# Performance work log

Measured on AMD Instinct MI355X. Metric: run time of the kernel, lower is better.

## Reference

```python
import jax, jax.numpy as jnp
import numpy as np

BN_EPS = 1e-5


def setup_inputs() -> dict:
    key = jax.random.key(0)
    ks = jax.random.split(key, 6)
    P, D_IN, H, N_NODES = 2_000_000, 3, 128, 20_000
    x = jax.random.normal(ks[0], (P, D_IN), dtype=jnp.float32)
    batch_idx = jax.random.randint(ks[1], (P,), 0, N_NODES, dtype=jnp.int64)
    W1 = jax.random.normal(ks[2], (D_IN, H), dtype=jnp.float32) * 0.5
    b1 = jax.random.normal(ks[3], (H,), dtype=jnp.float32) * 0.1
    gamma = jnp.ones((H,), dtype=jnp.float32)
    beta = jnp.zeros((H,), dtype=jnp.float32)
    running_mean = jnp.zeros((H,), dtype=jnp.float32)
    running_var = jnp.ones((H,), dtype=jnp.float32)
    W2 = jax.random.normal(ks[4], (H, H), dtype=jnp.float32) * (1.0 / np.sqrt(H))
    b2 = jax.random.normal(ks[5], (H,), dtype=jnp.float32) * 0.1
    return {"x": x, "batch_idx": batch_idx, "num_nodes": N_NODES,
            "W1": W1, "b1": b1, "gamma": gamma, "beta": beta,
            "running_mean": running_mean, "running_var": running_var,
            "W2": W2, "b2": b2}


def reference(x, batch_idx, num_nodes, W1, b1, gamma, beta,
              running_mean, running_var, W2, b2):
    # per-point MLP: Linear -> BatchNorm1d (eval: running stats) -> ReLU -> Linear -> ReLU
    h = x @ W1 + b1                                        # [P, H]
    h = (h - running_mean) * jax.lax.rsqrt(running_var + BN_EPS) * gamma + beta
    h = jax.nn.relu(h)
    h = jax.nn.relu(h @ W2 + b2)                            # [P, H], values >= 0
    # scatter_max by node; torch_scatter fills empty segments with 0,
    # and since h >= 0 post-ReLU, clamping the -inf fill to 0 is exact.
    node_feats = jax.ops.segment_max(h, batch_idx, num_segments=num_nodes)
    return jnp.maximum(node_feats, 0.0)                     # [num_nodes, H]
```

## Files before the change

kernel.cpp:

```cpp
#include <hip/hip_runtime.h>
#include <hip/hip_bf16.h>

#define H 128
#define TILE_PTS 32
#define ROW_STRIDE 136
#define NBLK 192
#define BT 1024
#define BSH 4
#define NPB (1 << BSH)
#define CAP 2048
#define RAWN (CAP + 32)
#define HBUF (TILE_PTS * ROW_STRIDE)

typedef __attribute__((ext_vector_type(8))) short short8;
typedef __attribute__((ext_vector_type(4))) float float4v;
typedef __attribute__((ext_vector_type(2))) float float2v;
typedef __attribute__((ext_vector_type(4))) int int4v;

static __device__ __forceinline__ unsigned short f2bf(float f) {
    unsigned u = __float_as_uint(f);
    unsigned r = (u + 0x7fffu + ((u >> 16) & 1u)) >> 16;
    return (unsigned short)r;
}
static __device__ __forceinline__ unsigned pkbf(float a, float b) {
    __hip_bfloat162 h = __float22bfloat162_rn(float2{a, b});
    return *reinterpret_cast<unsigned*>(&h);
}
static __device__ __forceinline__ unsigned short f2h(float f) {
    _Float16 h = (_Float16)f;
    unsigned short u;
    __builtin_memcpy(&u, &h, 2);
    return u;
}
static __device__ __forceinline__ float h2f(unsigned short us) {
    _Float16 h;
    __builtin_memcpy(&h, &us, 2);
    return (float)h;
}

__global__ __launch_bounds__(BT)
void scatter_slot(const int* __restrict__ bidx, const float* __restrict__ x,
                  const float* __restrict__ W2, unsigned short* __restrict__ W2T,
                  int* __restrict__ gcnt, uint2* __restrict__ xb,
                  int P, int nbuk) {
    extern __shared__ int lh[];
    const int b = blockIdx.x, t = threadIdx.x;
    for (int i = b * BT + t; i < H * H; i += NBLK * BT) {
        int n = i >> 7, k = i & 127;
        W2T[i] = f2bf(W2[k * H + n]);
    }
    for (int i = t; i < nbuk; i += BT) lh[i] = 0;
    __syncthreads();
    const int chunk4 = (((P + NBLK - 1) / NBLK) + 3) & ~3;
    const int lo = b * chunk4;
    const int hi = (lo + chunk4 < P) ? lo + chunk4 : P;
    for (int p4 = lo + 4 * t; p4 < hi; p4 += 4 * BT) {
        if (p4 + 4 <= hi) {
            int4v i4 = *(const int4v*)&bidx[p4];
            atomicAdd(&lh[i4.x >> BSH], 1);
            atomicAdd(&lh[i4.y >> BSH], 1);
            atomicAdd(&lh[i4.z >> BSH], 1);
            atomicAdd(&lh[i4.w >> BSH], 1);
        } else {
            for (int p = p4; p < hi; ++p) atomicAdd(&lh[bidx[p] >> BSH], 1);
        }
    }
    __syncthreads();
    for (int i = t; i < nbuk; i += BT) {
        int c = lh[i];
        lh[i] = (c > 0) ? atomicAdd(&gcnt[i], c) : 0;
    }
    __syncthreads();
    auto emit = [&](int idx, float x0, float x1, float x2) {
        int pos = atomicAdd(&lh[idx >> BSH], 1);
        if (pos < CAP) {
            uint2 r;
            r.x = (unsigned)f2h(x0) | ((unsigned)f2h(x1) << 16);
            r.y = (unsigned)f2h(x2) | ((unsigned)(idx & (NPB - 1)) << 16);
            xb[(size_t)(idx >> BSH) * CAP + pos] = r;
        }
    };
    for (int p4 = lo + 4 * t; p4 < hi; p4 += 4 * BT) {
        if (p4 + 4 <= hi) {
            int4v i4 = *(const int4v*)&bidx[p4];
            float4v xa = *(const float4v*)(x + (size_t)p4 * 3);
            float4v xbv = *(const float4v*)(x + (size_t)p4 * 3 + 4);
            float4v xc = *(const float4v*)(x + (size_t)p4 * 3 + 8);
            emit(i4.x, xa[0], xa[1], xa[2]);
            emit(i4.y, xa[3], xbv[0], xbv[1]);
            emit(i4.z, xbv[2], xbv[3], xc[0]);
            emit(i4.w, xc[1], xc[2], xc[3]);
        } else {
            for (int p = p4; p < hi; ++p)
                emit(bidx[p], x[p * 3 + 0], x[p * 3 + 1], x[p * 3 + 2]);
        }
    }
}

__global__ __launch_bounds__(256, 4)
void node_kernel9(const uint2* __restrict__ xb, const int* __restrict__ gcnt,
                  const float* __restrict__ W1, const float* __restrict__ b1,
                  const float* __restrict__ gamma, const float* __restrict__ beta,
                  const float* __restrict__ rmean, const float* __restrict__ rvar,
                  const unsigned short* __restrict__ W2T, const float* __restrict__ b2,
                  float* __restrict__ out, int N)
{
    __shared__ __align__(16) unsigned short pool[2 * HBUF];
    __shared__ __align__(16) uint2 srt[RAWN];
    __shared__ int basec[NPB + 1];
    __shared__ int cur[NPB];

    const int bk   = blockIdx.x;
    const int t    = threadIdx.x;
    const int lane = t & 63;
    const int wave = t >> 6;
    const int g  = t & 15;
    const int q  = t >> 4;
    const int c0 = g * 8;

    float2v w1f2[3][4], b1f2[4];
    #pragma unroll
    for (int jp = 0; jp < 4; ++jp) {
        #pragma unroll
        for (int e = 0; e < 2; ++e) {
            int c = c0 + 2 * jp + e;
            float sc = gamma[c] * rsqrtf(rvar[c] + 1e-5f);
            w1f2[0][jp][e] = W1[0 * H + c] * sc;
            w1f2[1][jp][e] = W1[1 * H + c] * sc;
            w1f2[2][jp][e] = W1[2 * H + c] * sc;
            b1f2[jp][e]    = (b1[c] - rmean[c]) * sc + beta[c];
        }
    }

    const int bn = lane & 15;
    const int kq = (lane >> 4) * 8;
    short8 bfrag[2][4];
    float  b2v[2];
    #pragma unroll
    for (int nt = 0; nt < 2; ++nt) {
        const int nn = wave * 32 + nt * 16 + bn;
        b2v[nt] = b2[nn];
        #pragma unroll
        for (int kk = 0; kk < 4; ++kk)
            bfrag[nt][kk] = *(const short8*)&W2T[nn * H + kk * 32 + kq];
    }

    uint2* raw = (uint2*)pool;
    int n_b = gcnt[bk];
    if (n_b > CAP) n_b = CAP;
    const uint2* src = xb + (size_t)bk * CAP;
    for (int p = t; p < n_b; p += 256) raw[p] = src[p];
    if (t < NPB) cur[t] = 0;
    __syncthreads();
    for (int p = t; p < n_b; p += 256)
        atomicAdd(&cur[raw[p].y >> 16], 1);
    __syncthreads();
    if (t == 0) {
        int run = 0;
        #pragma unroll
        for (int i = 0; i < NPB; ++i) { int c = cur[i]; basec[i] = run; run += c; }
        basec[NPB] = run;
    }
    __syncthreads();
    if (t < NPB) cur[t] = basec[t];
    __syncthreads();
    for (int p = t; p < n_b; p += 256) {
        uint2 r = raw[p];
        int pos = atomicAdd(&cur[r.y >> 16], 1);
        srt[pos] = r;
    }
    for (int p = n_b + t; p < n_b + TILE_PTS; p += 256)
        if (p < RAWN) srt[p] = uint2{0u, 0u};
    __syncthreads();

    const float4v zero4 = {0.f, 0.f, 0.f, 0.f};
    const float NEG_INF = -__builtin_inff();
    const float2v zero2 = {0.f, 0.f};
    const int nodebase = bk << BSH;
    const int nlocal = (N - nodebase < NPB) ? (N - nodebase) : NPB;

    const int st0 = q * ROW_STRIDE + c0;
    const int st1 = (q + 16) * ROW_STRIDE + c0;
    const int ar  = bn * ROW_STRIDE + kq;

    #define STAGE_PT(r, hs, so)                                            \
    {                                                                      \
        float x0 = h2f((unsigned short)((r).x & 0xffffu));                 \
        float x1 = h2f((unsigned short)((r).x >> 16));                     \
        float x2 = h2f((unsigned short)((r).y & 0xffffu));                 \
        float2v a0 = {x0, x0}, a1 = {x1, x1}, a2 = {x2, x2};               \
        int4v pk;                                                          \
        _Pragma("unroll")                                                  \
        for (int jp = 0; jp < 4; ++jp) {                                   \
            float2v hh = b1f2[jp];                                         \
            hh = __builtin_elementwise_fma(a0, w1f2[0][jp], hh);           \
            hh = __builtin_elementwise_fma(a1, w1f2[1][jp], hh);           \
            hh = __builtin_elementwise_fma(a2, w1f2[2][jp], hh);           \
            hh = __builtin_elementwise_max(hh, zero2);                     \
            pk[jp] = (int)pkbf(hh[0], hh[1]);                              \
        }                                                                  \
        *(int4v*)(void*)&(hs)[so] = pk;                                    \
    }

    for (int j = 0; j < nlocal; ++j) {
        const int startj = basec[j];
        const int n      = basec[j + 1] - startj;
        const int ntiles = (n + TILE_PTS - 1) >> 5;

        float2v vm0 = {NEG_INF, NEG_INF};
        float2v vm1 = {NEG_INF, NEG_INF};

        if (ntiles > 0) {
            unsigned short* hb = pool;
            unsigned short* hs = pool + HBUF;
            {
                uint2 r0 = srt[startj + q];
                uint2 r1 = srt[startj + q + 16];
                STAGE_PT(r0, hb, st0);
                STAGE_PT(r1, hb, st1);
            }
            __syncthreads();

            for (int tile = 0; tile < ntiles; ++tile) {
                const int tb = tile * TILE_PTS;
                const bool have = (tile + 1 < ntiles);

                uint2 n0, n1;
                if (have) {
                    n0 = srt[startj + tb + TILE_PTS + q];
                    n1 = srt[startj + tb + TILE_PTS + 16 + q];
                }

                float4v acc00, acc01, acc10, acc11;
                {
                    short8 a0v = *(const short8*)(const void*)&hb[ar];
                    short8 a1v = *(const short8*)(const void*)&hb[ar + 16 * ROW_STRIDE];
                    acc00 = __builtin_amdgcn_mfma_f32_16x16x32_bf16(a0v, bfrag[0][0], zero4, 0, 0, 0);
                    acc01 = __builtin_amdgcn_mfma_f32_16x16x32_bf16(a0v, bfrag[1][0], zero4, 0, 0, 0);
                    acc10 = __builtin_amdgcn_mfma_f32_16x16x32_bf16(a1v, bfrag[0][0], zero4, 0, 0, 0);
                    acc11 = __builtin_amdgcn_mfma_f32_16x16x32_bf16(a1v, bfrag[1][0], zero4, 0, 0, 0);
                }
                #pragma unroll
                for (int kk = 1; kk < 4; ++kk) {
                    short8 a0v = *(const short8*)(const void*)&hb[ar + kk * 32];
                    short8 a1v = *(const short8*)(const void*)&hb[ar + 16 * ROW_STRIDE + kk * 32];
                    acc00 = __builtin_amdgcn_mfma_f32_16x16x32_bf16(a0v, bfrag[0][kk], acc00, 0, 0, 0);
                    acc01 = __builtin_amdgcn_mfma_f32_16x16x32_bf16(a0v, bfrag[1][kk], acc01, 0, 0, 0);
                    acc10 = __builtin_amdgcn_mfma_f32_16x16x32_bf16(a1v, bfrag[0][kk], acc10, 0, 0, 0);
                    acc11 = __builtin_amdgcn_mfma_f32_16x16x32_bf16(a1v, bfrag[1][kk], acc11, 0, 0, 0);
                }

                if (have) {
                    STAGE_PT(n0, hs, st0);
                    STAGE_PT(n1, hs, st1);
                }

                if (tb + TILE_PTS <= n) {
                    vm0 = __builtin_elementwise_max(vm0, float2v{acc00[0], acc00[1]});
                    vm0 = __builtin_elementwise_max(vm0, float2v{acc00[2], acc00[3]});
                    vm0 = __builtin_elementwise_max(vm0, float2v{acc10[0], acc10[1]});
                    vm0 = __builtin_elementwise_max(vm0, float2v{acc10[2], acc10[3]});
                    vm1 = __builtin_elementwise_max(vm1, float2v{acc01[0], acc01[1]});
                    vm1 = __builtin_elementwise_max(vm1, float2v{acc01[2], acc01[3]});
                    vm1 = __builtin_elementwise_max(vm1, float2v{acc11[0], acc11[1]});
                    vm1 = __builtin_elementwise_max(vm1, float2v{acc11[2], acc11[3]});
                } else {
                    const int r0base = (lane >> 4) * 4;
                    #pragma unroll
                    for (int r = 0; r < 4; ++r) {
                        const bool v0 = (tb + r0base + r) < n;
                        const bool v1 = (tb + 16 + r0base + r) < n;
                        vm0[r & 1] = fmaxf(vm0[r & 1], v0 ? acc00[r] : NEG_INF);
                        vm1[r & 1] = fmaxf(vm1[r & 1], v0 ? acc01[r] : NEG_INF);
                        vm0[r & 1] = fmaxf(vm0[r & 1], v1 ? acc10[r] : NEG_INF);
                        vm1[r & 1] = fmaxf(vm1[r & 1], v1 ? acc11[r] : NEG_INF);
                    }
                }
                __syncthreads();
                unsigned short* tmp = hb; hb = hs; hs = tmp;
            }
        }

        float vmax0 = fmaxf(vm0[0], vm0[1]);
        float vmax1 = fmaxf(vm1[0], vm1[1]);
        vmax0 = fmaxf(vmax0, __shfl_xor(vmax0, 16, 64));
        vmax0 = fmaxf(vmax0, __shfl_xor(vmax0, 32, 64));
        vmax1 = fmaxf(vmax1, __shfl_xor(vmax1, 16, 64));
        vmax1 = fmaxf(vmax1, __shfl_xor(vmax1, 32, 64));
        if (lane < 16) {
            float* orow = out + (size_t)(nodebase + j) * H + wave * 32;
            orow[lane]      = fmaxf(vmax0 + b2v[0], 0.f);
            orow[16 + lane] = fmaxf(vmax1 + b2v[1], 0.f);
        }
    }
    #undef STAGE_PT
}

__global__ void histB_kernel(const int* __restrict__ bidx, int* __restrict__ counts, int P) {
    int p = blockIdx.x * 256 + threadIdx.x;
    if (p < P) atomicAdd(&counts[bidx[p]], 1);
}
__global__ __launch_bounds__(1024)
void scanB_kernel(const int* __restrict__ counts, int* __restrict__ starts,
                  int* __restrict__ cursor, int N) {
    __shared__ int sums[1024];
    const int t = threadIdx.x;
    const int chunk = (N + 1023) >> 10;
    const int lo = t * chunk;
    const int hi = (lo + chunk < N) ? lo + chunk : N;
    int s = 0;
    for (int i = lo; i < hi; ++i) s += counts[i];
    sums[t] = s;
    __syncthreads();
    #pragma unroll
    for (int off = 1; off < 1024; off <<= 1) {
        int a = (t >= off) ? sums[t - off] : 0;
        __syncthreads();
        sums[t] += a;
        __syncthreads();
    }
    int run = sums[t] - s;
    for (int i = lo; i < hi; ++i) { starts[i] = run; cursor[i] = run; run += counts[i]; }
    if (t == 1023) starts[N] = sums[1023];
}
__global__ void scatterB_kernel(const int* __restrict__ bidx, const float* __restrict__ x,
                                int* __restrict__ cursor, uint2* __restrict__ xs, int P) {
    int p = blockIdx.x * 256 + threadIdx.x;
    if (p < P) {
        int pos = atomicAdd(&cursor[bidx[p]], 1);
        uint2 r;
        r.x = (unsigned)f2h(x[p * 3 + 0]) | ((unsigned)f2h(x[p * 3 + 1]) << 16);
        r.y = (unsigned)f2h(x[p * 3 + 2]);
        xs[pos] = r;
    }
}
__global__ void convw2_kernel(const float* __restrict__ W2, unsigned short* __restrict__ W2T) {
    int i = blockIdx.x * 256 + threadIdx.x;
    if (i < H * H) {
        int n = i >> 7, k = i & 127;
        W2T[i] = f2bf(W2[k * H + n]);
    }
}

__global__ __launch_bounds__(256, 4)
void node_kernelB(const uint2* __restrict__ xs,
                  const int*   __restrict__ starts,
                  const float* __restrict__ W1, const float* __restrict__ b1,
                  const float* __restrict__ gamma, const float* __restrict__ beta,
                  const float* __restrict__ rmean, const float* __restrict__ rvar,
                  const unsigned short* __restrict__ W2T, const float* __restrict__ b2,
                  float* __restrict__ out, int N)
{
    __shared__ __align__(16) unsigned short h1s[2][TILE_PTS * ROW_STRIDE];
    const int t = threadIdx.x, lane = t & 63, wave = t >> 6;
    const int g = t & 15, q = t >> 4, c0 = g * 8;
    float2v w1f2[3][4], b1f2[4];
    #pragma unroll
    for (int jp = 0; jp < 4; ++jp)
        #pragma unroll
        for (int e = 0; e < 2; ++e) {
            int c = c0 + 2 * jp + e;
            float sc = gamma[c] * rsqrtf(rvar[c] + 1e-5f);
            w1f2[0][jp][e] = W1[0 * H + c] * sc;
            w1f2[1][jp][e] = W1[1 * H + c] * sc;
            w1f2[2][jp][e] = W1[2 * H + c] * sc;
            b1f2[jp][e]    = (b1[c] - rmean[c]) * sc + beta[c];
        }
    const int bn = lane & 15, kq = (lane >> 4) * 8;
    short8 bfrag[2][4]; float b2v[2];
    #pragma unroll
    for (int nt = 0; nt < 2; ++nt) {
        const int nn = wave * 32 + nt * 16 + bn;
        b2v[nt] = b2[nn];
        #pragma unroll
        for (int kk = 0; kk < 4; ++kk)
            bfrag[nt][kk] = *(const short8*)&W2T[nn * H + kk * 32 + kq];
    }
    const float4v zero4 = {0.f, 0.f, 0.f, 0.f};
    const float NEG_INF = -__builtin_inff();
    const float2v zero2 = {0.f, 0.f};
    for (int node = blockIdx.x; node < N; node += gridDim.x) {
        const int start = starts[node];
        const int n = starts[node + 1] - start;
        const int ntiles = (n + TILE_PTS - 1) >> 5;
        float2v vmax2[2];
        vmax2[0] = float2v{NEG_INF, NEG_INF};
        vmax2[1] = float2v{NEG_INF, NEG_INF};
        auto loadx = [&](int tb, float xv[2][3]) {
            #pragma unroll
            for (int i = 0; i < 2; ++i) {
                uint2 r = xs[start + tb + q + 16 * i];
                xv[i][0] = h2f((unsigned short)(r.x & 0xffffu));
                xv[i][1] = h2f((unsigned short)(r.x >> 16));
                xv[i][2] = h2f((unsigned short)(r.y & 0xffffu));
            }
        };
        auto stage = [&](const float xv[2][3], unsigned short* buf) {
            #pragma unroll
            for (int i = 0; i < 2; ++i) {
                const int pl = q + 16 * i;
                float2v a0 = {xv[i][0], xv[i][0]};
                float2v a1 = {xv[i][1], xv[i][1]};
                float2v a2 = {xv[i][2], xv[i][2]};
                int4v pk;
                #pragma unroll
                for (int jp = 0; jp < 4; ++jp) {
                    float2v h = b1f2[jp];
                    h = __builtin_elementwise_fma(a0, w1f2[0][jp], h);
                    h = __builtin_elementwise_fma(a1, w1f2[1][jp], h);
                    h = __builtin_elementwise_fma(a2, w1f2[2][jp], h);
                    h = __builtin_elementwise_max(h, zero2);
                    pk[jp] = (int)pkbf(h[0], h[1]);
                }
                *(int4v*)(void*)&buf[pl * ROW_STRIDE + c0] = pk;
            }
        };
        if (ntiles > 0) {
            float xv[2][3];
            loadx(0, xv);
            stage(xv, h1s[0]);
            __syncthreads();
            int pb = 0;
            for (int tile = 0; tile < ntiles; ++tile) {
                const int tb = tile * TILE_PTS;
                const bool havenext = (tile + 1 < ntiles);
                float nx[2][3];
                if (havenext) loadx(tb + TILE_PTS, nx);
                float4v acc[2][2];
                const unsigned short* hb = h1s[pb];
                {
                    short8 a0 = *(const short8*)&hb[bn * ROW_STRIDE + kq];
                    short8 a1 = *(const short8*)&hb[(16 + bn) * ROW_STRIDE + kq];
                    #pragma unroll
                    for (int nt = 0; nt < 2; ++nt) {
                        acc[0][nt] = __builtin_amdgcn_mfma_f32_16x16x32_bf16(a0, bfrag[nt][0], zero4, 0, 0, 0);
                        acc[1][nt] = __builtin_amdgcn_mfma_f32_16x16x32_bf16(a1, bfrag[nt][0], zero4, 0, 0, 0);
                    }
                }
                #pragma unroll
                for (int kk = 1; kk < 4; ++kk) {
                    short8 a0 = *(const short8*)&hb[bn * ROW_STRIDE + kk * 32 + kq];
                    short8 a1 = *(const short8*)&hb[(16 + bn) * ROW_STRIDE + kk * 32 + kq];
                    #pragma unroll
                    for (int nt = 0; nt < 2; ++nt) {
                        acc[0][nt] = __builtin_amdgcn_mfma_f32_16x16x32_bf16(a0, bfrag[nt][kk], acc[0][nt], 0, 0, 0);
                        acc[1][nt] = __builtin_amdgcn_mfma_f32_16x16x32_bf16(a1, bfrag[nt][kk], acc[1][nt], 0, 0, 0);
                    }
                }
                if (havenext) stage(nx, h1s[pb ^ 1]);
                if (tb + TILE_PTS <= n) {
                    #pragma unroll
                    for (int ps = 0; ps < 2; ++ps)
                        #pragma unroll
                        for (int nt = 0; nt < 2; ++nt) {
                            vmax2[nt] = __builtin_elementwise_max(vmax2[nt],
                                          float2v{acc[ps][nt][0], acc[ps][nt][1]});
                            vmax2[nt] = __builtin_elementwise_max(vmax2[nt],
                                          float2v{acc[ps][nt][2], acc[ps][nt][3]});
                        }
                } else {
                    #pragma unroll
                    for (int ps = 0; ps < 2; ++ps)
                        #pragma unroll
                        for (int r = 0; r < 4; ++r) {
                            const int pl = ps * 16 + (lane >> 4) * 4 + r;
                            const bool valid = (tb + pl) < n;
                            vmax2[0][r & 1] = fmaxf(vmax2[0][r & 1], valid ? acc[ps][0][r] : NEG_INF);
                            vmax2[1][r & 1] = fmaxf(vmax2[1][r & 1], valid ? acc[ps][1][r] : NEG_INF);
                        }
                }
                __syncthreads();
                pb ^= 1;
            }
        }
        float vmax0 = fmaxf(vmax2[0][0], vmax2[0][1]);
        float vmax1 = fmaxf(vmax2[1][0], vmax2[1][1]);
        vmax0 = fmaxf(vmax0, __shfl_xor(vmax0, 16, 64));
        vmax0 = fmaxf(vmax0, __shfl_xor(vmax0, 32, 64));
        vmax1 = fmaxf(vmax1, __shfl_xor(vmax1, 16, 64));
        vmax1 = fmaxf(vmax1, __shfl_xor(vmax1, 32, 64));
        if (lane < 16) {
            float* orow = out + (size_t)node * H + wave * 32;
            orow[lane]      = fmaxf(vmax0 + b2v[0], 0.f);
            orow[16 + lane] = fmaxf(vmax1 + b2v[1], 0.f);
        }
    }
}

extern "C" void kernel_launch(void* const* d_in, const int* in_sizes, int n_in,
                              void* d_out, int out_size, void* d_ws, size_t ws_size,
                              hipStream_t stream) {
    const float* x     = (const float*)d_in[0];
    const int*   bidx  = (const int*)  d_in[1];
    const float* W1    = (const float*)d_in[3];
    const float* b1    = (const float*)d_in[4];
    const float* gamma = (const float*)d_in[5];
    const float* beta  = (const float*)d_in[6];
    const float* rmean = (const float*)d_in[7];
    const float* rvar  = (const float*)d_in[8];
    const float* W2    = (const float*)d_in[9];
    const float* b2    = (const float*)d_in[10];
    float* out = (float*)d_out;

    const int P = in_sizes[1];
    const int N = out_size / H;
    const int nbuk = (N + NPB - 1) >> BSH;

    const size_t szW2T = 32768;
    const size_t szG   = (size_t)4 * ((nbuk + 63) & ~63);
    const size_t szXb  = (size_t)8 * ((size_t)CAP * nbuk + 64);
    const size_t needA = szW2T + szG + szXb + 256;
    const size_t lds1  = (size_t)4 * nbuk;

    char* w = (char*)d_ws;

    if (lds1 <= 60000 && ws_size >= needA) {
        unsigned short* W2T = (unsigned short*)w;
        int* gcnt = (int*)(w + szW2T);
        uint2* xb = (uint2*)(w + szW2T + szG);

        hipMemsetAsync(gcnt, 0, (size_t)nbuk * sizeof(int), stream);
        scatter_slot<<<NBLK, BT, lds1, stream>>>(bidx, x, W2, W2T, gcnt, xb, P, nbuk);
        node_kernel9<<<nbuk, 256, 0, stream>>>(xb, gcnt, W1, b1, gamma, beta,
                                               rmean, rvar, W2T, b2, out, N);
        return;
    }

    const int Npad = (N + 63) & ~63;
    const size_t szStarts = (size_t)4 * (Npad + 64);
    const size_t szCnt    = (size_t)4 * Npad;
    const size_t szRec    = (size_t)8 * (P + 64);
    const size_t needB    = szStarts + szW2T + 2 * szCnt + szRec + 256;
    if (ws_size >= needB) {
        int* starts = (int*)w;
        unsigned short* W2T = (unsigned short*)(w + szStarts);
        int* counts = (int*)(w + szStarts + szW2T);
        int* cursor = (int*)(w + szStarts + szW2T + szCnt);
        uint2* xs   = (uint2*)(w + szStarts + szW2T + 2 * szCnt);

        hipMemsetAsync(counts, 0, (size_t)N * sizeof(int), stream);
        const int pblocks = (P + 255) / 256;
        const int grid = (N < 2048) ? N : 2048;
        convw2_kernel<<<(H * H + 255) / 256, 256, 0, stream>>>(W2, W2T);
        histB_kernel<<<pblocks, 256, 0, stream>>>(bidx, counts, P);
        scanB_kernel<<<1, 1024, 0, stream>>>(counts, starts, cursor, N);
        scatterB_kernel<<<pblocks, 256, 0, stream>>>(bidx, x, cursor, xs, P);
        node_kernelB<<<grid, 256, 0, stream>>>(xs, starts, W1, b1, gamma, beta,
                                               rmean, rvar, W2T, b2, out, N);
    }
}
```

Baseline: 230.8 us.

## Switch layer math to fp16, drop LDS sort buffer, raise occupancy and scatter blocks

Computes the first layer in packed fp16 FMAs and runs the second-layer MFMAs in f16 instead of bf16, with W2 converted to half. The per-bucket sorted point array moves out of LDS and is written back into the global bucket, which cuts LDS use so the launch bound can ask for 8 blocks per CU. The scatter kernel grid grows from 192 to 512 blocks. Reading sorted points from global memory adds latency and needs a threadfence, and the zero-padding past the bucket end is gone, so tail tiles may read stale bucket data.

```diff
diff --git a/kernel.cpp b/kernel.cpp
--- a/kernel.cpp
+++ b/kernel.cpp
@@ -4,18 +4,19 @@
 #define H 128
 #define TILE_PTS 32
 #define ROW_STRIDE 136
-#define NBLK 192
+#define NBLK 512
 #define BT 1024
 #define BSH 4
 #define NPB (1 << BSH)
 #define CAP 2048
-#define RAWN (CAP + 32)
 #define HBUF (TILE_PTS * ROW_STRIDE)
 
 typedef __attribute__((ext_vector_type(8))) short short8;
 typedef __attribute__((ext_vector_type(4))) float float4v;
 typedef __attribute__((ext_vector_type(2))) float float2v;
 typedef __attribute__((ext_vector_type(4))) int int4v;
+typedef _Float16 half8 __attribute__((ext_vector_type(8)));
+typedef _Float16 half2 __attribute__((ext_vector_type(2)));
 
 static __device__ __forceinline__ unsigned short f2bf(float f) {
     unsigned u = __float_as_uint(f);
@@ -47,7 +48,7 @@
     const int b = blockIdx.x, t = threadIdx.x;
     for (int i = b * BT + t; i < H * H; i += NBLK * BT) {
         int n = i >> 7, k = i & 127;
-        W2T[i] = f2bf(W2[k * H + n]);
+        W2T[i] = f2h(W2[k * H + n]);
     }
     for (int i = t; i < nbuk; i += BT) lh[i] = 0;
     __syncthreads();
@@ -97,16 +98,15 @@
     }
 }
 
-__global__ __launch_bounds__(256, 4)
-void node_kernel9(const uint2* __restrict__ xb, const int* __restrict__ gcnt,
-                  const float* __restrict__ W1, const float* __restrict__ b1,
-                  const float* __restrict__ gamma, const float* __restrict__ beta,
-                  const float* __restrict__ rmean, const float* __restrict__ rvar,
-                  const unsigned short* __restrict__ W2T, const float* __restrict__ b2,
-                  float* __restrict__ out, int N)
+__global__ __launch_bounds__(256, 8)
+void node_kernel10(uint2* __restrict__ xb, const int* __restrict__ gcnt,
+                   const float* __restrict__ W1, const float* __restrict__ b1,
+                   const float* __restrict__ gamma, const float* __restrict__ beta,
+                   const float* __restrict__ rmean, const float* __restrict__ rvar,
+                   const unsigned short* __restrict__ W2T, const float* __restrict__ b2,
+                   float* __restrict__ out, int N)
 {
     __shared__ __align__(16) unsigned short pool[2 * HBUF];
-    __shared__ __align__(16) uint2 srt[RAWN];
     __shared__ int basec[NPB + 1];
     __shared__ int cur[NPB];
 
@@ -118,38 +118,38 @@
     const int q  = t >> 4;
     const int c0 = g * 8;
 
-    float2v w1f2[3][4], b1f2[4];
+    half2 w1h[3][4], b1h[4];
     #pragma unroll
     for (int jp = 0; jp < 4; ++jp) {
         #pragma unroll
         for (int e = 0; e < 2; ++e) {
             int c = c0 + 2 * jp + e;
             float sc = gamma[c] * rsqrtf(rvar[c] + 1e-5f);
-            w1f2[0][jp][e] = W1[0 * H + c] * sc;
-            w1f2[1][jp][e] = W1[1 * H + c] * sc;
-            w1f2[2][jp][e] = W1[2 * H + c] * sc;
-            b1f2[jp][e]    = (b1[c] - rmean[c]) * sc + beta[c];
+            w1h[0][jp][e] = (_Float16)(W1[0 * H + c] * sc);
+            w1h[1][jp][e] = (_Float16)(W1[1 * H + c] * sc);
+            w1h[2][jp][e] = (_Float16)(W1[2 * H + c] * sc);
+            b1h[jp][e]    = (_Float16)((b1[c] - rmean[c]) * sc + beta[c]);
         }
     }
 
     const int bn = lane & 15;
     const int kq = (lane >> 4) * 8;
-    short8 bfrag[2][4];
-    float  b2v[2];
+    half8 bfrag[2][4];
+    float b2v[2];
     #pragma unroll
     for (int nt = 0; nt < 2; ++nt) {
         const int nn = wave * 32 + nt * 16 + bn;
         b2v[nt] = b2[nn];
         #pragma unroll
         for (int kk = 0; kk < 4; ++kk)
-            bfrag[nt][kk] = *(const short8*)&W2T[nn * H + kk * 32 + kq];
+            bfrag[nt][kk] = *(const half8*)(const void*)&W2T[nn * H + kk * 32 + kq];
     }
 
     uint2* raw = (uint2*)pool;
     int n_b = gcnt[bk];
     if (n_b > CAP) n_b = CAP;
-    const uint2* src = xb + (size_t)bk * CAP;
-    for (int p = t; p < n_b; p += 256) raw[p] = src[p];
+    uint2* bucket = xb + (size_t)bk * CAP;
+    for (int p = t; p < n_b; p += 256) raw[p] = bucket[p];
     if (t < NPB) cur[t] = 0;
     __syncthreads();
     for (int p = t; p < n_b; p += 256)
@@ -167,15 +167,14 @@
     for (int p = t; p < n_b; p += 256) {
         uint2 r = raw[p];
         int pos = atomicAdd(&cur[r.y >> 16], 1);
-        srt[pos] = r;
-    }
-    for (int p = n_b + t; p < n_b + TILE_PTS; p += 256)
-        if (p < RAWN) srt[p] = uint2{0u, 0u};
+        bucket[pos] = r;
+    }
+    __threadfence();
     __syncthreads();
 
     const float4v zero4 = {0.f, 0.f, 0.f, 0.f};
     const float NEG_INF = -__builtin_inff();
-    const float2v zero2 = {0.f, 0.f};
+    const half2 zero2h = {(_Float16)0.f, (_Float16)0.f};
     const int nodebase = bk << BSH;
     const int nlocal = (N - nodebase < NPB) ? (N - nodebase) : NPB;
 
@@ -185,22 +184,26 @@
 
     #define STAGE_PT(r, hs, so)                                            \
     {                                                                      \
-        float x0 = h2f((unsigned short)((r).x & 0xffffu));                 \
-        float x1 = h2f((unsigned short)((r).x >> 16));                     \
-        float x2 = h2f((unsigned short)((r).y & 0xffffu));                 \
-        float2v a0 = {x0, x0}, a1 = {x1, x1}, a2 = {x2, x2};               \
+        half2 a0 = __builtin_bit_cast(half2,                               \
+            __builtin_amdgcn_perm(0u, (r).x, 0x01000100u));                \
+        half2 a1 = __builtin_bit_cast(half2,                               \
+            __builtin_amdgcn_perm(0u, (r).x, 0x03020302u));                \
+        half2 a2 = __builtin_bit_cast(half2,                               \
+            __builtin_amdgcn_perm(0u, (r).y, 0x01000100u));                \
         int4v pk;                                                          \
         _Pragma("unroll")                                                  \
         for (int jp = 0; jp < 4; ++jp) {                                   \
-            float2v hh = b1f2[jp];                                         \
-            hh = __builtin_elementwise_fma(a0, w1f2[0][jp], hh);           \
-            hh = __builtin_elementwise_fma(a1, w1f2[1][jp], hh);           \
-            hh = __builtin_elementwise_fma(a2, w1f2[2][jp], hh);           \
-            hh = __builtin_elementwise_max(hh, zero2);                     \
-            pk[jp] = (int)pkbf(hh[0], hh[1]);                              \
+            half2 hh = b1h[jp];                                            \
+            hh = __builtin_elementwise_fma(a0, w1h[0][jp], hh);            \
+            hh = __builtin_elementwise_fma(a1, w1h[1][jp], hh);            \
+            hh = __builtin_elementwise_fma(a2, w1h[2][jp], hh);            \
+            hh = __builtin_elementwise_max(hh, zero2h);                    \
+            pk[jp] = __builtin_bit_cast(int, hh);                          \
         }                                                                  \
         *(int4v*)(void*)&(hs)[so] = pk;                                    \
     }
+
+    const uint2* srtb = bucket;
 
     for (int j = 0; j < nlocal; ++j) {
         const int startj = basec[j];
@@ -214,8 +217,8 @@
             unsigned short* hb = pool;
             unsigned short* hs = pool + HBUF;
             {
-                uint2 r0 = srt[startj + q];
-                uint2 r1 = srt[startj + q + 16];
+                uint2 r0 = srtb[startj + q];
+                uint2 r1 = srtb[startj + q + 16];
                 STAGE_PT(r0, hb, st0);
                 STAGE_PT(r1, hb, st1);
             }
@@ -227,27 +230,27 @@
 
                 uint2 n0, n1;
                 if (have) {
-                    n0 = srt[startj + tb + TILE_PTS + q];
-                    n1 = srt[startj + tb + TILE_PTS + 16 + q];
+                    n0 = srtb[startj + tb + TILE_PTS + q];
+                    n1 = srtb[startj + tb + TILE_PTS + 16 + q];
                 }
 
                 float4v acc00, acc01, acc10, acc11;
                 {
-                    short8 a0v = *(const short8*)(const void*)&hb[ar];
-                    short8 a1v = *(const short8*)(const void*)&hb[ar + 16 * ROW_STRIDE];
-                    acc00 = __builtin_amdgcn_mfma_f32_16x16x32_bf16(a0v, bfrag[0][0], zero4, 0, 0, 0);
-                    acc01 = __builtin_amdgcn_mfma_f32_16x16x32_bf16(a0v, bfrag[1][0], zero4, 0, 0, 0);
-                    acc10 = __builtin_amdgcn_mfma_f32_16x16x32_bf16(a1v, bfrag[0][0], zero4, 0, 0, 0);
-                    acc11 = __builtin_amdgcn_mfma_f32_16x16x32_bf16(a1v, bfrag[1][0], zero4, 0, 0, 0);
+                    half8 a0v = *(const half8*)(const void*)&hb[ar];
+                    half8 a1v = *(const half8*)(const void*)&hb[ar + 16 * ROW_STRIDE];
+                    acc00 = __builtin_amdgcn_mfma_f32_16x16x32_f16(a0v, bfrag[0][0], zero4, 0, 0, 0);
+                    acc01 = __builtin_amdgcn_mfma_f32_16x16x32_f16(a0v, bfrag[1][0], zero4, 0, 0, 0);
+                    acc10 = __builtin_amdgcn_mfma_f32_16x16x32_f16(a1v, bfrag[0][0], zero4, 0, 0, 0);
+                    acc11 = __builtin_amdgcn_mfma_f32_16x16x32_f16(a1v, bfrag[1][0], zero4, 0, 0, 0);
                 }
                 #pragma unroll
                 for (int kk = 1; kk < 4; ++kk) {
-                    short8 a0v = *(const short8*)(const void*)&hb[ar + kk * 32];
-                    short8 a1v = *(const short8*)(const void*)&hb[ar + 16 * ROW_STRIDE + kk * 32];
-                    acc00 = __builtin_amdgcn_mfma_f32_16x16x32_bf16(a0v, bfrag[0][kk], acc00, 0, 0, 0);
-                    acc01 = __builtin_amdgcn_mfma_f32_16x16x32_bf16(a0v, bfrag[1][kk], acc01, 0, 0, 0);
-                    acc10 = __builtin_amdgcn_mfma_f32_16x16x32_bf16(a1v, bfrag[0][kk], acc10, 0, 0, 0);
-                    acc11 = __builtin_amdgcn_mfma_f32_16x16x32_bf16(a1v, bfrag[1][kk], acc11, 0, 0, 0);
+                    half8 a0v = *(const half8*)(const void*)&hb[ar + kk * 32];
+                    half8 a1v = *(const half8*)(const void*)&hb[ar + 16 * ROW_STRIDE + kk * 32];
+                    acc00 = __builtin_amdgcn_mfma_f32_16x16x32_f16(a0v, bfrag[0][kk], acc00, 0, 0, 0);
+                    acc01 = __builtin_amdgcn_mfma_f32_16x16x32_f16(a0v, bfrag[1][kk], acc01, 0, 0, 0);
+                    acc10 = __builtin_amdgcn_mfma_f32_16x16x32_f16(a1v, bfrag[0][kk], acc10, 0, 0, 0);
+                    acc11 = __builtin_amdgcn_mfma_f32_16x16x32_f16(a1v, bfrag[1][kk], acc11, 0, 0, 0);
                 }
 
                 if (have) {
@@ -521,8 +524,8 @@
 
         hipMemsetAsync(gcnt, 0, (size_t)nbuk * sizeof(int), stream);
         scatter_slot<<<NBLK, BT, lds1, stream>>>(bidx, x, W2, W2T, gcnt, xb, P, nbuk);
-        node_kernel9<<<nbuk, 256, 0, stream>>>(xb, gcnt, W1, b1, gamma, beta,
-                                               rmean, rvar, W2T, b2, out, N);
+        node_kernel10<<<nbuk, 256, 0, stream>>>(xb, gcnt, W1, b1, gamma, beta,
+                                                rmean, rvar, W2T, b2, out, N);
         return;
     }
 
```

New measurement: 642.0 us. +178.1%, slower.
